# Optimization experiments

Hardware: AMD Instinct MI355X
Metric: run time of the kernel (lower is better)

Reference implementation:

```python
import jax, jax.numpy as jnp
import numpy as np

B, K, D = 131072, 1024, 128  # batch, codebook size, code dim


def setup_inputs() -> dict:
    key = jax.random.key(0)
    k1, k2 = jax.random.split(key)
    z_e = jax.random.normal(k1, (B, D), dtype=jnp.float32)
    # nn.Embedding weight init: uniform(-1/K, 1/K) as in TactileVQ.__init__
    codebook = jax.random.uniform(k2, (K, D), dtype=jnp.float32,
                                  minval=-1.0 / K, maxval=1.0 / K)
    return {"z_e": z_e, "codebook": codebook}


def reference(z_e, codebook):
    """TactileVQ forward: cdist(p=2) -> argmin -> codebook gather -> commitment MSE.
    Squared distances share the same argmin as euclidean cdist, so we use the
    expansion ||z||^2 - 2 z.E^T + ||E||^2 and never take a sqrt.
    """
    z_sq = jnp.sum(z_e * z_e, axis=-1, keepdims=True)          # [B, 1]
    e_sq = jnp.sum(codebook * codebook, axis=-1)               # [K]
    # [B, K] squared distances (monotone transform of cdist p=2)
    d2 = z_sq - 2.0 * jnp.einsum('bd,kd->bk', z_e, codebook) + e_sq
    encoding_indices = jnp.argmin(d2, axis=-1)                 # [B] int
    z_q = codebook[encoding_indices]                           # [B, D] gather
    commitment_loss = jnp.mean(
        (z_q - jax.lax.stop_gradient(z_e)) ** 2)               # mse vs detached z_e
    return z_q, commitment_loss, encoding_indices
```

## Files before the change

### kernel.cpp

```cpp
#include <hip/hip_runtime.h>
#include <math.h>

#define BN 131072
#define KN 1024
#define DN 128
#define GCODES 64
#define NGRP (KN / GCODES)

#define EROWS 64
#define EBLK (BN / EROWS)

#define ROWS 64
#define NBLK (BN / ROWS)

#define TAMB 2.5e-4f
#define CANARY 0.01f

typedef __attribute__((ext_vector_type(8))) short s16x8;
typedef __attribute__((ext_vector_type(4))) short s16x4;
typedef __attribute__((ext_vector_type(4))) float f32x4;

__device__ __forceinline__ unsigned short f2bf(float f) {
    const unsigned int u = __float_as_uint(f);
    return (unsigned short)((u + 0x7fffu + ((u >> 16) & 1u)) >> 16);
}
__device__ __forceinline__ float bf2f(unsigned short s) {
    return __uint_as_float(((unsigned int)s) << 16);
}
__device__ __forceinline__ void cvt4(const float4 v, s16x4& h4, s16x4& l4) {
    const unsigned short h0 = f2bf(v.x), h1 = f2bf(v.y), h2 = f2bf(v.z), h3 = f2bf(v.w);
    h4[0] = (short)h0; h4[1] = (short)h1; h4[2] = (short)h2; h4[3] = (short)h3;
    l4[0] = (short)f2bf(v.x - bf2f(h0));
    l4[1] = (short)f2bf(v.y - bf2f(h1));
    l4[2] = (short)f2bf(v.z - bf2f(h2));
    l4[3] = (short)f2bf(v.w - bf2f(h3));
}
__device__ __forceinline__ void cvt8(const float4 v0, const float4 v1,
                                     s16x8& h, s16x8& l) {
    s16x4 h0, l0, h1, l1;
    cvt4(v0, h0, l0); cvt4(v1, h1, l1);
    h[0]=h0[0]; h[1]=h0[1]; h[2]=h0[2]; h[3]=h0[3];
    h[4]=h1[0]; h[5]=h1[1]; h[6]=h1[2]; h[7]=h1[3];
    l[0]=l0[0]; l[1]=l0[1]; l[2]=l0[2]; l[3]=l0[3];
    l[4]=l1[0]; l[5]=l1[1]; l[6]=l1[2]; l[7]=l1[3];
}

__global__ __launch_bounds__(256) void esq_kernel(const float* __restrict__ cb,
                                                  float* __restrict__ esq) {
    int k = blockIdx.x * 256 + threadIdx.x;
    if (k >= KN) return;
    const float* row = cb + (size_t)k * DN;
    float r[8];
#pragma unroll
    for (int j = 0; j < 8; ++j) r[j] = __fmul_rn(row[j], row[j]);
#pragma unroll
    for (int i = 8; i < DN; i += 8) {
#pragma unroll
        for (int j = 0; j < 8; ++j)
            r[j] = __fadd_rn(r[j], __fmul_rn(row[i + j], row[i + j]));
    }
    esq[k] = __fadd_rn(
        __fadd_rn(__fadd_rn(r[0], r[1]), __fadd_rn(r[2], r[3])),
        __fadd_rn(__fadd_rn(r[4], r[5]), __fadd_rn(r[6], r[7])));
}

__global__ __launch_bounds__(256) void cvt_kernel(const float* __restrict__ cb,
                                                  unsigned short* __restrict__ pl) {
    const int t = blockIdx.x * 256 + threadIdx.x;
    const int g = t >> 10, rem = t & 1023;
    const int m = rem >> 6, c = rem & 63;
    const float* src = cb + ((size_t)(g * 64 + c)) * DN + m * 8;
    const float4 v0 = *reinterpret_cast<const float4*>(src);
    const float4 v1 = *reinterpret_cast<const float4*>(src + 4);
    s16x8 h, l;
    cvt8(v0, v1, h, l);
    unsigned short* hb = pl + (size_t)g * 16384 + (m * 64 + c) * 8;
    *reinterpret_cast<s16x8*>(hb)        = h;
    *reinterpret_cast<s16x8*>(hb + 8192) = l;
}

__global__ __launch_bounds__(256) void cvtT_kernel(const float* __restrict__ cb,
                                                   float* __restrict__ cbT) {
    const int idx = blockIdx.x * 256 + threadIdx.x;
    const int d = idx >> 10, k = idx & 1023;
    cbT[idx] = cb[(size_t)k * DN + d];
}

__global__ __launch_bounds__(256) void zprep_kernel(const float* __restrict__ z,
                                                    unsigned short* __restrict__ zp,
                                                    float* __restrict__ zsq) {
    const int row = blockIdx.x * 256 + threadIdx.x;
    const float* zr = z + (size_t)row * DN;
    const int gt = row >> 4, rr = row & 15;
    unsigned short* hb = zp + (size_t)gt * 4096 + rr * 8;
    float a8[8];
#pragma unroll
    for (int m = 0; m < 16; ++m) {
        const float4 v0 = *reinterpret_cast<const float4*>(zr + m * 8);
        const float4 v1 = *reinterpret_cast<const float4*>(zr + m * 8 + 4);
        s16x8 h, l;
        cvt8(v0, v1, h, l);
        *reinterpret_cast<s16x8*>(hb + m * 128)        = h;
        *reinterpret_cast<s16x8*>(hb + 2048 + m * 128) = l;
        if (m == 0) {
            a8[0] = __fmul_rn(v0.x, v0.x); a8[1] = __fmul_rn(v0.y, v0.y);
            a8[2] = __fmul_rn(v0.z, v0.z); a8[3] = __fmul_rn(v0.w, v0.w);
            a8[4] = __fmul_rn(v1.x, v1.x); a8[5] = __fmul_rn(v1.y, v1.y);
            a8[6] = __fmul_rn(v1.z, v1.z); a8[7] = __fmul_rn(v1.w, v1.w);
        } else {
            a8[0] = __fadd_rn(a8[0], __fmul_rn(v0.x, v0.x));
            a8[1] = __fadd_rn(a8[1], __fmul_rn(v0.y, v0.y));
            a8[2] = __fadd_rn(a8[2], __fmul_rn(v0.z, v0.z));
            a8[3] = __fadd_rn(a8[3], __fmul_rn(v0.w, v0.w));
            a8[4] = __fadd_rn(a8[4], __fmul_rn(v1.x, v1.x));
            a8[5] = __fadd_rn(a8[5], __fmul_rn(v1.y, v1.y));
            a8[6] = __fadd_rn(a8[6], __fmul_rn(v1.z, v1.z));
            a8[7] = __fadd_rn(a8[7], __fmul_rn(v1.w, v1.w));
        }
    }
    zsq[row] = __fadd_rn(
        __fadd_rn(__fadd_rn(a8[0], a8[1]), __fadd_rn(a8[2], a8[3])),
        __fadd_rn(__fadd_rn(a8[4], a8[5]), __fadd_rn(a8[6], a8[7])));
}

__device__ __forceinline__ float exact_d2_g(const float* __restrict__ z,
                                            const float* __restrict__ cb,
                                            const int grow, const int k,
                                            const float zsq, const float ek) {
    const float* zr = z + (size_t)grow * DN;
    const float* cr = cb + (size_t)k * DN;
    float dot = 0.0f;
#pragma unroll 4
    for (int j = 0; j < 32; ++j) {
        const float4 zv = *reinterpret_cast<const float4*>(zr + j * 4);
        const float4 cv = *reinterpret_cast<const float4*>(cr + j * 4);
        dot = __fmaf_rn(zv.x, cv.x, dot);
        dot = __fmaf_rn(zv.y, cv.y, dot);
        dot = __fmaf_rn(zv.z, cv.z, dot);
        dot = __fmaf_rn(zv.w, cv.w, dot);
    }
    return __fadd_rn(__fsub_rn(zsq, __fmul_rn(2.0f, dot)), ek);
}

__device__ __forceinline__ void tile_compute(const s16x8 (&ch)[4][4],
                                             const s16x8 (&cl)[4][4],
                                             const s16x8 (&zh)[4],
                                             const s16x8 (&zl)[4],
                                             const float (&ekv)[16],
                                             const int kbase, const int r0,
                                             float4* __restrict__ pq,
                                             const int l15, const int l4h) {
    f32x4 acc[4];
#pragma unroll
    for (int ct = 0; ct < 4; ++ct) acc[ct] = (f32x4){0.0f, 0.0f, 0.0f, 0.0f};
    __builtin_amdgcn_s_setprio(1);
#pragma unroll
    for (int ks = 0; ks < 4; ++ks) {
#pragma unroll
        for (int ct = 0; ct < 4; ++ct) {
            acc[ct] = __builtin_amdgcn_mfma_f32_16x16x32_bf16(ch[ct][ks], zh[ks], acc[ct], 0, 0, 0);
            acc[ct] = __builtin_amdgcn_mfma_f32_16x16x32_bf16(cl[ct][ks], zh[ks], acc[ct], 0, 0, 0);
            acc[ct] = __builtin_amdgcn_mfma_f32_16x16x32_bf16(ch[ct][ks], zl[ks], acc[ct], 0, 0, 0);
        }
    }
    __builtin_amdgcn_s_setprio(0);
    float b1 = INFINITY, b2 = INFINITY, b3 = INFINITY;
    int   i1 = 0, i2 = 0;
#pragma unroll
    for (int ct = 0; ct < 4; ++ct) {
#pragma unroll
        for (int e = 0; e < 4; ++e) {
            const float sc = __fmaf_rn(-2.0f, acc[ct][e], ekv[ct * 4 + e]);
            const int   kk = kbase + ct * 16 + l4h * 4 + e;
            const bool lt1 = sc < b1;
            const bool lt2 = sc < b2;
            const float nb3 = __builtin_amdgcn_fmed3f(sc, b2, b3);
            const float nb2 = __builtin_amdgcn_fmed3f(sc, b1, b2);
            i2 = lt1 ? i1 : (lt2 ? kk : i2);
            b3 = nb3;
            b2 = nb2;
            b1 = fminf(sc, b1);
            i1 = lt1 ? kk : i1;
        }
    }
#pragma unroll
    for (int st = 16; st < 64; st <<= 1) {
        const float ob1 = __shfl_xor(b1, st);
        const int   oi1 = __shfl_xor(i1, st);
        const float ob2 = __shfl_xor(b2, st);
        const int   oi2 = __shfl_xor(i2, st);
        const float ob3 = __shfl_xor(b3, st);
        float v1, v2, v3; int j1, j2;
        if (ob1 < b1) {
            v1 = ob1; j1 = oi1;
            if (b1 < ob2) { v2 = b1;  j2 = i1;  v3 = fminf(b2, ob2); }
            else          { v2 = ob2; j2 = oi2; v3 = fminf(b1, ob3); }
        } else {
            v1 = b1; j1 = i1;
            if (ob1 < b2) { v2 = ob1; j2 = oi1; v3 = fminf(ob2, b2); }
            else          { v2 = b2;  j2 = i2;  v3 = fminf(ob1, b3); }
        }
        b1 = v1; i1 = j1; b2 = v2; i2 = j2; b3 = v3;
    }
    if (l4h == 0) {
        float4 q;
        q.x = b1; q.y = b2; q.z = b3;
        q.w = __int_as_float((i2 << 16) | i1);
        pq[r0 + l15] = q;
    }
}

__device__ __forceinline__ void tile_load_zp(const unsigned short* __restrict__ zb,
                                             s16x8 (&zh)[4], s16x8 (&zl)[4]) {
#pragma unroll
    for (int ks = 0; ks < 4; ++ks) {
        zh[ks] = *reinterpret_cast<const s16x8*>(zb + ks * 512);
        zl[ks] = *reinterpret_cast<const s16x8*>(zb + 2048 + ks * 512);
    }
}

__global__ __launch_bounds__(256, 2) void vq_score_pre(const unsigned short* __restrict__ zp,
                                                       const unsigned short* __restrict__ planes,
                                                       const float* __restrict__ esq,
                                                       float4* __restrict__ pquad) {
    const int tid  = threadIdx.x;
    const int lane = tid & 63;
    const int w    = tid >> 6;
    const int l15  = lane & 15;
    const int l4h  = lane >> 4;
    const int sliceW = blockIdx.x >> 8;
    const int chunk2 = blockIdx.x & 255;
    const int sub    = sliceW * 4 + w;
    const int kbase  = sub * 64;

    s16x8 ch[4][4], cl[4][4];
    {
        const unsigned short* gp = planes + (size_t)sub * 16384;
#pragma unroll
        for (int ks = 0; ks < 4; ++ks)
#pragma unroll
            for (int ct = 0; ct < 4; ++ct) {
                const int off = ((((ks * 4 + l4h) << 6) + (ct << 4) + l15) << 3);
                ch[ct][ks] = *reinterpret_cast<const s16x8*>(gp + off);
                cl[ct][ks] = *reinterpret_cast<const s16x8*>(gp + 8192 + off);
            }
    }
    float ekv[16];
#pragma unroll
    for (int ct = 0; ct < 4; ++ct)
#pragma unroll
        for (int e = 0; e < 4; ++e)
            ekv[ct * 4 + e] = esq[kbase + ct * 16 + l4h * 4 + e];

    const int cbase = chunk2 * 32;
    const int rbase = chunk2 * 512;
    float4* pq = pquad + (size_t)sub * BN;
    const unsigned short* zpl = zp + l4h * 128 + l15 * 8;

    s16x8 hA[4], lA[4], hB[4], lB[4];
    tile_load_zp(zpl + (size_t)cbase * 4096, hA, lA);
#pragma unroll 1
    for (int t = 0; t < 32; t += 2) {
        tile_load_zp(zpl + (size_t)(cbase + t + 1) * 4096, hB, lB);
        tile_compute(ch, cl, hA, lA, ekv, kbase, rbase + t * 16, pq, l15, l4h);
        const int tn = (t + 2 < 32) ? t + 2 : 31;
        tile_load_zp(zpl + (size_t)(cbase + tn) * 4096, hA, lA);
        tile_compute(ch, cl, hB, lB, ekv, kbase, rbase + (t + 1) * 16, pq, l15, l4h);
    }
}

__global__ __launch_bounds__(256, 2) void vq_score(const float* __restrict__ z,
                                                   const unsigned short* __restrict__ planes,
                                                   const float* __restrict__ esq,
                                                   float4* __restrict__ pquad) {
    const int tid  = threadIdx.x;
    const int lane = tid & 63;
    const int w    = tid >> 6;
    const int l15  = lane & 15;
    const int l4h  = lane >> 4;
    const int sliceW = blockIdx.x >> 7;
    const int chunk  = blockIdx.x & 127;
    const int sub    = sliceW * 4 + w;
    const int kbase  = sub * 64;

    s16x8 ch[4][4], cl[4][4];
    {
        const unsigned short* gp = planes + (size_t)sub * 16384;
#pragma unroll
        for (int ks = 0; ks < 4; ++ks)
#pragma unroll
            for (int ct = 0; ct < 4; ++ct) {
                const int off = ((((ks * 4 + l4h) << 6) + (ct << 4) + l15) << 3);
                ch[ct][ks] = *reinterpret_cast<const s16x8*>(gp + off);
                cl[ct][ks] = *reinterpret_cast<const s16x8*>(gp + 8192 + off);
            }
    }
    float ekv[16];
#pragma unroll
    for (int ct = 0; ct < 4; ++ct)
#pragma unroll
        for (int e = 0; e < 4; ++e)
            ekv[ct * 4 + e] = esq[kbase + ct * 16 + l4h * 4 + e];

    const int rbase = chunk * 1024;
    float4* pq = pquad + (size_t)sub * BN;

#pragma unroll 1
    for (int t = 0; t < 64; ++t) {
        const int r0 = rbase + t * 16;
        s16x8 zh[4], zl[4];
#pragma unroll
        for (int ks = 0; ks < 4; ++ks) {
            const float* src = z + (size_t)(r0 + l15) * DN + ks * 32 + l4h * 8;
            const float4 v0 = *reinterpret_cast<const float4*>(src);
            const float4 v1 = *reinterpret_cast<const float4*>(src + 4);
            cvt8(v0, v1, zh[ks], zl[ks]);
        }
        tile_compute(ch, cl, zh, zl, ekv, kbase, r0, pq, l15, l4h);
    }
}

template <bool HZ>
__global__ __launch_bounds__(256, 2) void vq_merge3(const float* __restrict__ z,
                                                    const float* __restrict__ cb,
                                                    const float* __restrict__ esq,
                                                    const float* __restrict__ zsqArr,
                                                    const float4* __restrict__ pquad,
                                                    int* __restrict__ rmeta,
                                                    int* __restrict__ rlist,
                                                    float* __restrict__ out) {
    const int tid = threadIdx.x;
    const int r   = blockIdx.x * 256 + tid;

    float zsq;
    if constexpr (HZ) {
        zsq = zsqArr[r];
    } else {
        const float* zr = z + (size_t)r * DN;
        float a8[8];
#pragma unroll
        for (int c = 0; c < 32; ++c) {
            const float4 v = *reinterpret_cast<const float4*>(zr + c * 4);
            const int t0 = 4 * (c & 1);
            if (c < 2) {
                a8[t0 + 0] = __fmul_rn(v.x, v.x);
                a8[t0 + 1] = __fmul_rn(v.y, v.y);
                a8[t0 + 2] = __fmul_rn(v.z, v.z);
                a8[t0 + 3] = __fmul_rn(v.w, v.w);
            } else {
                a8[t0 + 0] = __fadd_rn(a8[t0 + 0], __fmul_rn(v.x, v.x));
                a8[t0 + 1] = __fadd_rn(a8[t0 + 1], __fmul_rn(v.y, v.y));
                a8[t0 + 2] = __fadd_rn(a8[t0 + 2], __fmul_rn(v.z, v.z));
                a8[t0 + 3] = __fadd_rn(a8[t0 + 3], __fmul_rn(v.w, v.w));
            }
        }
        zsq = __fadd_rn(
            __fadd_rn(__fadd_rn(a8[0], a8[1]), __fadd_rn(a8[2], a8[3])),
            __fadd_rn(__fadd_rn(a8[4], a8[5]), __fadd_rn(a8[6], a8[7])));
    }

    float B1 = INFINITY, B2 = INFINITY, B3 = INFINITY;
    int   I1 = 0, I2 = 0;
#pragma unroll
    for (int half = 0; half < 2; ++half) {
        float4 q[8];
#pragma unroll
        for (int s = 0; s < 8; ++s)
            q[s] = pquad[(size_t)(half * 8 + s) * BN + r];
#pragma unroll
        for (int s = 0; s < 8; ++s) {
            const int ii = __float_as_int(q[s].w);
            const int j1 = ii & 0xffff, j2 = ii >> 16;
            {
                const float sc = q[s].x;
                const bool lt1 = sc < B1;
                const bool lt2 = sc < B2;
                const float nB3 = __builtin_amdgcn_fmed3f(sc, B2, B3);
                const float nB2 = __builtin_amdgcn_fmed3f(sc, B1, B2);
                I2 = lt1 ? I1 : (lt2 ? j1 : I2);
                B3 = nB3;
                B2 = nB2;
                B1 = fminf(sc, B1);
                I1 = lt1 ? j1 : I1;
            }
            {
                const float sc = q[s].y;
                const bool l2 = sc < B2;
                const float nB3 = __builtin_amdgcn_fmed3f(sc, B2, B3);
                I2 = l2 ? j2 : I2;
                B3 = nB3;
                B2 = fminf(sc, B2);
            }
            B3 = fminf(B3, q[s].z);
        }
    }

    int win = I1;
    if (B3 - B1 <= TAMB) {
        const int p = atomicAdd(&rmeta[0], 1);
        rlist[p] = r;
    } else if (B2 - B1 <= TAMB) {
        const float da = exact_d2_g(z, cb, r, I1, zsq, esq[I1]);
        const float db = exact_d2_g(z, cb, r, I2, zsq, esq[I2]);
        if (da < db) win = I1;
        else if (db < da) win = I2;
        else win = (I1 < I2) ? I1 : I2;
    }
    out[(size_t)BN * DN + 1 + r] = (float)win;

    if ((tid & 63) == 0) {
        const float d2x  = exact_d2_g(z, cb, r, I1, zsq, esq[I1]);
        const float pred = __fadd_rn(zsq, B1);
        if (fabsf(pred - d2x) > CANARY) atomicExch(&rmeta[1], 1);
    }
}

template <bool HZ>
__global__ __launch_bounds__(256, 2) void vq_rescue2(const float* __restrict__ z,
                                                     const float* __restrict__ cbT,
                                                     const float* __restrict__ esq,
                                                     const float* __restrict__ zsqArr,
                                                     const int* __restrict__ rmeta,
                                                     const int* __restrict__ rlist,
                                                     float* __restrict__ out) {
    const int lane = threadIdx.x & 63;
    const int wid  = blockIdx.x * 4 + (threadIdx.x >> 6);
    const int nw   = gridDim.x * 4;
    const int n    = rmeta[0];
    const int flag = rmeta[1];
    const int total = flag ? BN : n;

    for (int ii = wid; ii < total; ii += nw) {
        const int row = flag ? ii : rlist[ii];
        float zsq;
        if constexpr (HZ) {
            zsq = zsqArr[row];
        } else {
            const float* zr0 = z + (size_t)row * DN;
            float a8[8];
#pragma unroll
            for (int c = 0; c < 32; ++c) {
                const float4 v = *reinterpret_cast<const float4*>(zr0 + c * 4);
                const int t0 = 4 * (c & 1);
                if (c < 2) {
                    a8[t0 + 0] = __fmul_rn(v.x, v.x);
                    a8[t0 + 1] = __fmul_rn(v.y, v.y);
                    a8[t0 + 2] = __fmul_rn(v.z, v.z);
                    a8[t0 + 3] = __fmul_rn(v.w, v.w);
                } else {
                    a8[t0 + 0] = __fadd_rn(a8[t0 + 0], __fmul_rn(v.x, v.x));
                    a8[t0 + 1] = __fadd_rn(a8[t0 + 1], __fmul_rn(v.y, v.y));
                    a8[t0 + 2] = __fadd_rn(a8[t0 + 2], __fmul_rn(v.z, v.z));
                    a8[t0 + 3] = __fadd_rn(a8[t0 + 3], __fmul_rn(v.w, v.w));
                }
            }
            zsq = __fadd_rn(
                __fadd_rn(__fadd_rn(a8[0], a8[1]), __fadd_rn(a8[2], a8[3])),
                __fadd_rn(__fadd_rn(a8[4], a8[5]), __fadd_rn(a8[6], a8[7])));
        }

        const float* zr = z + (size_t)row * DN;
        float acc[16];
#pragma unroll
        for (int c = 0; c < 16; ++c) acc[c] = 0.0f;
#pragma unroll 1
        for (int d = 0; d < DN; ++d) {
            const float zd = zr[d];
            const float* cd = cbT + (size_t)d * KN + lane;
#pragma unroll
            for (int c = 0; c < 16; ++c)
                acc[c] = __fmaf_rn(zd, cd[c * 64], acc[c]);
        }
        float best = INFINITY; int bi = 0;
#pragma unroll
        for (int c = 0; c < 16; ++c) {
            const int k = c * 64 + lane;
            const float d2 = __fadd_rn(__fsub_rn(zsq, __fmul_rn(2.0f, acc[c])),
                                       esq[k]);
            if (d2 < best) { best = d2; bi = k; }
        }
#pragma unroll
        for (int m = 1; m < 64; m <<= 1) {
            const float ob  = __shfl_xor(best, m);
            const int   obi = __shfl_xor(bi, m);
            if (ob < best || (ob == best && obi < bi)) { best = ob; bi = obi; }
        }
        if (lane == 0) out[(size_t)BN * DN + 1 + row] = (float)bi;
    }
}

__global__ __launch_bounds__(256, 4) void vq_epilogue(const float* __restrict__ z,
                                                      const float* __restrict__ cb,
                                                      float* __restrict__ out,
                                                      double* __restrict__ partials) {
    __shared__ int sidx[EROWS];
    __shared__ double sls[256];
    const int tid  = threadIdx.x;
    const int row0 = blockIdx.x * EROWS;

    if (tid < EROWS)
        sidx[tid] = (int)out[(size_t)BN * DN + 1 + row0 + tid];
    __syncthreads();

    double ls = 0.0;
    const int j = tid & 31;
#pragma unroll
    for (int half = 0; half < 2; ++half) {
        float4 zb[4], cv[4];
        int rr[4];
#pragma unroll
        for (int u = 0; u < 4; ++u) {
            const int it = half * 4 + u;
            rr[u] = it * 8 + (tid >> 5);
            zb[u] = *reinterpret_cast<const float4*>(
                z + (size_t)(row0 + rr[u]) * DN + j * 4);
            cv[u] = *reinterpret_cast<const float4*>(
                cb + (size_t)sidx[rr[u]] * DN + j * 4);
        }
#pragma unroll
        for (int u = 0; u < 4; ++u) {
            *reinterpret_cast<float4*>(out + (size_t)(row0 + rr[u]) * DN + j * 4) = cv[u];
            const float d0 = __fsub_rn(cv[u].x, zb[u].x);
            const float d1 = __fsub_rn(cv[u].y, zb[u].y);
            const float d2e = __fsub_rn(cv[u].z, zb[u].z);
            const float d3 = __fsub_rn(cv[u].w, zb[u].w);
            ls += (double)__fmul_rn(d0, d0);
            ls += (double)__fmul_rn(d1, d1);
            ls += (double)__fmul_rn(d2e, d2e);
            ls += (double)__fmul_rn(d3, d3);
        }
    }
    sls[tid] = ls;
    __syncthreads();
    for (int s = 128; s > 0; s >>= 1) {
        if (tid < s) sls[tid] += sls[tid + s];
        __syncthreads();
    }
    if (tid == 0) partials[blockIdx.x] = sls[0];
}

#define UPD(s, sc, kk) { \
    const bool lt1 = (sc) < b1v[s]; \
    const bool lt2 = (sc) < b2v[s]; \
    const bool lt3 = (sc) < b3v[s]; \
    b3v[s] = lt2 ? b2v[s] : (lt3 ? (sc) : b3v[s]); \
    b2v[s] = lt1 ? b1v[s] : (lt2 ? (sc) : b2v[s]); \
    i2v[s] = lt1 ? i1v[s] : (lt2 ? (kk) : i2v[s]); \
    b1v[s] = lt1 ? (sc) : b1v[s]; \
    i1v[s] = lt1 ? (kk) : i1v[s]; }

__global__ __launch_bounds__(256, 2) void vq_lds(const float* __restrict__ z,
                                                 const float* __restrict__ cb,
                                                 const float* __restrict__ esq,
                                                 float* __restrict__ out,
                                                 double* __restrict__ partials) {
    __shared__ __align__(16) short cbS[2][16384];
    __shared__ __align__(16) float sEsq[KN];
    __shared__ float  szsq[ROWS];
    __shared__ float  sB1[2][ROWS], sB2[2][ROWS], sB3[2][ROWS];
    __shared__ int    sI1[2][ROWS], sI2[2][ROWS];
    __shared__ int    sbidx[ROWS];
    __shared__ int    t2list[ROWS], t3list[ROWS];
    __shared__ int    t2n, t3n;
    __shared__ double sls[256];

    const int tid  = threadIdx.x;
    const int lane = tid & 63;
    const int w    = tid >> 6;
    const int l15  = lane & 15;
    const int l4h  = lane >> 4;
    const int wr   = w >> 1;
    const int wc   = w & 1;
    const int row0 = blockIdx.x * ROWS;

    if (tid == 0) { t2n = 0; t3n = 0; }
#pragma unroll
    for (int i = 0; i < 4; ++i) sEsq[i * 256 + tid] = esq[i * 256 + tid];

    float4 stg[8];
#pragma unroll
    for (int i = 0; i < 4; ++i) {
        const int mc = i * 256 + tid, m = mc >> 6, c = mc & 63;
        const float* src = cb + ((size_t)c) * DN + m * 8;
        stg[2 * i]     = *reinterpret_cast<const float4*>(src);
        stg[2 * i + 1] = *reinterpret_cast<const float4*>(src + 4);
    }

    if (tid < ROWS) {
        const float* zr = z + (size_t)(row0 + tid) * DN;
        float rr[8];
#pragma unroll
        for (int c = 0; c < 32; ++c) {
            const float4 v = *reinterpret_cast<const float4*>(zr + c * 4);
            const int t0 = 4 * (c & 1);
            if (c < 2) {
                rr[t0 + 0] = __fmul_rn(v.x, v.x);
                rr[t0 + 1] = __fmul_rn(v.y, v.y);
                rr[t0 + 2] = __fmul_rn(v.z, v.z);
                rr[t0 + 3] = __fmul_rn(v.w, v.w);
            } else {
                rr[t0 + 0] = __fadd_rn(rr[t0 + 0], __fmul_rn(v.x, v.x));
                rr[t0 + 1] = __fadd_rn(rr[t0 + 1], __fmul_rn(v.y, v.y));
                rr[t0 + 2] = __fadd_rn(rr[t0 + 2], __fmul_rn(v.z, v.z));
                rr[t0 + 3] = __fadd_rn(rr[t0 + 3], __fmul_rn(v.w, v.w));
            }
        }
        szsq[tid] = __fadd_rn(
            __fadd_rn(__fadd_rn(rr[0], rr[1]), __fadd_rn(rr[2], rr[3])),
            __fadd_rn(__fadd_rn(rr[4], rr[5]), __fadd_rn(rr[6], rr[7])));
    }

    {
        short* dst = &cbS[0][0];
#pragma unroll
        for (int i = 0; i < 4; ++i) {
            const int mc = i * 256 + tid, m = mc >> 6, c = mc & 63;
            s16x4 h0, l0, h1, l1;
            cvt4(stg[2 * i], h0, l0); cvt4(stg[2 * i + 1], h1, l1);
            short* hb = dst + (m * 64 + c) * 8;
            *reinterpret_cast<s16x4*>(hb)     = h0;
            *reinterpret_cast<s16x4*>(hb + 4) = h1;
            short* lb = hb + 8192;
            *reinterpret_cast<s16x4*>(lb)     = l0;
            *reinterpret_cast<s16x4*>(lb + 4) = l1;
        }
    }

    s16x8 zha[2][4], zla[2][4];
#pragma unroll
    for (int rt = 0; rt < 2; ++rt) {
#pragma unroll
        for (int ks = 0; ks < 4; ++ks) {
            const int rl = row0 + wr * 32 + rt * 16 + l15;
            const float* src = z + (size_t)rl * DN + ks * 32 + l4h * 8;
            const float4 v0 = *reinterpret_cast<const float4*>(src);
            const float4 v1 = *reinterpret_cast<const float4*>(src + 4);
            cvt8(v0, v1, zha[rt][ks], zla[rt][ks]);
        }
    }
    __syncthreads();

    float b1v[8], b2v[8], b3v[8]; int i1v[8], i2v[8];
#pragma unroll
    for (int s = 0; s < 8; ++s) {
        b1v[s] = INFINITY; b2v[s] = INFINITY; b3v[s] = INFINITY;
        i1v[s] = 0; i2v[s] = 0;
    }

    for (int g = 0; g < NGRP; ++g) {
        const int buf = g & 1;
        if (g < NGRP - 1) {
            const int gb = (g + 1) * GCODES;
#pragma unroll
            for (int i = 0; i < 4; ++i) {
                const int mc = i * 256 + tid, m = mc >> 6, c = mc & 63;
                const float* src = cb + ((size_t)(gb + c)) * DN + m * 8;
                stg[2 * i]     = *reinterpret_cast<const float4*>(src);
                stg[2 * i + 1] = *reinterpret_cast<const float4*>(src + 4);
            }
        }

        f32x4 acc[2][2];
#pragma unroll
        for (int rt = 0; rt < 2; ++rt)
#pragma unroll
            for (int ct = 0; ct < 2; ++ct)
                acc[rt][ct] = (f32x4){0.0f, 0.0f, 0.0f, 0.0f};

#pragma unroll
        for (int ks = 0; ks < 4; ++ks) {
            const int b0 = (((ks * 4 + l4h) << 6) + (wc << 5) + l15) << 3;
            const s16x8 bh0 = *reinterpret_cast<const s16x8*>(&cbS[buf][b0]);
            const s16x8 bl0 = *reinterpret_cast<const s16x8*>(&cbS[buf][8192 + b0]);
            const s16x8 bh1 = *reinterpret_cast<const s16x8*>(&cbS[buf][b0 + 128]);
            const s16x8 bl1 = *reinterpret_cast<const s16x8*>(&cbS[buf][8192 + b0 + 128]);
            acc[0][0] = __builtin_amdgcn_mfma_f32_16x16x32_bf16(zha[0][ks], bh0, acc[0][0], 0, 0, 0);
            acc[0][0] = __builtin_amdgcn_mfma_f32_16x16x32_bf16(zla[0][ks], bh0, acc[0][0], 0, 0, 0);
            acc[0][0] = __builtin_amdgcn_mfma_f32_16x16x32_bf16(zha[0][ks], bl0, acc[0][0], 0, 0, 0);
            acc[1][0] = __builtin_amdgcn_mfma_f32_16x16x32_bf16(zha[1][ks], bh0, acc[1][0], 0, 0, 0);
            acc[1][0] = __builtin_amdgcn_mfma_f32_16x16x32_bf16(zla[1][ks], bh0, acc[1][0], 0, 0, 0);
            acc[1][0] = __builtin_amdgcn_mfma_f32_16x16x32_bf16(zha[1][ks], bl0, acc[1][0], 0, 0, 0);
            acc[0][1] = __builtin_amdgcn_mfma_f32_16x16x32_bf16(zha[0][ks], bh1, acc[0][1], 0, 0, 0);
            acc[0][1] = __builtin_amdgcn_mfma_f32_16x16x32_bf16(zla[0][ks], bh1, acc[0][1], 0, 0, 0);
            acc[0][1] = __builtin_amdgcn_mfma_f32_16x16x32_bf16(zha[0][ks], bl1, acc[0][1], 0, 0, 0);
            acc[1][1] = __builtin_amdgcn_mfma_f32_16x16x32_bf16(zha[1][ks], bh1, acc[1][1], 0, 0, 0);
            acc[1][1] = __builtin_amdgcn_mfma_f32_16x16x32_bf16(zla[1][ks], bh1, acc[1][1], 0, 0, 0);
            acc[1][1] = __builtin_amdgcn_mfma_f32_16x16x32_bf16(zha[1][ks], bl1, acc[1][1], 0, 0, 0);
        }

#pragma unroll
        for (int ct = 0; ct < 2; ++ct) {
            const int k = g * GCODES + wc * 32 + ct * 16 + l15;
            const float ek = sEsq[k];
#pragma unroll
            for (int rt = 0; rt < 2; ++rt) {
#pragma unroll
                for (int e = 0; e < 4; ++e) {
                    const float sc = __fmaf_rn(-2.0f, acc[rt][ct][e], ek);
                    UPD(rt * 4 + e, sc, k)
                }
            }
        }

        if (g < NGRP - 1) {
            short* dst = &cbS[buf ^ 1][0];
#pragma unroll
            for (int i = 0; i < 4; ++i) {
                const int mc = i * 256 + tid, m = mc >> 6, c = mc & 63;
                s16x4 h0, l0, h1, l1;
                cvt4(stg[2 * i], h0, l0); cvt4(stg[2 * i + 1], h1, l1);
                short* hb = dst + (m * 64 + c) * 8;
                *reinterpret_cast<s16x4*>(hb)     = h0;
                *reinterpret_cast<s16x4*>(hb + 4) = h1;
                short* lb = hb + 8192;
                *reinterpret_cast<s16x4*>(lb)     = l0;
                *reinterpret_cast<s16x4*>(lb + 4) = l1;
            }
        }
        __syncthreads();
    }

#pragma unroll
    for (int st = 1; st < 16; st <<= 1) {
#pragma unroll
        for (int s = 0; s < 8; ++s) {
            const float ob1 = __shfl_xor(b1v[s], st);
            const int   oi1 = __shfl_xor(i1v[s], st);
            const float ob2 = __shfl_xor(b2v[s], st);
            const int   oi2 = __shfl_xor(i2v[s], st);
            const float ob3 = __shfl_xor(b3v[s], st);
            float v1, v2, v3; int j1, j2;
            if (ob1 < b1v[s]) {
                v1 = ob1; j1 = oi1;
                if (b1v[s] < ob2) { v2 = b1v[s]; j2 = i1v[s]; v3 = fminf(b2v[s], ob2); }
                else              { v2 = ob2;    j2 = oi2;    v3 = fminf(b1v[s], ob3); }
            } else {
                v1 = b1v[s]; j1 = i1v[s];
                if (ob1 < b2v[s]) { v2 = ob1;    j2 = oi1;    v3 = fminf(ob2, b2v[s]); }
                else              { v2 = b2v[s]; j2 = i2v[s]; v3 = fminf(ob1, b3v[s]); }
            }
            b1v[s] = v1; i1v[s] = j1; b2v[s] = v2; i2v[s] = j2; b3v[s] = v3;
        }
    }
    if (l15 == 0) {
#pragma unroll
        for (int s = 0; s < 8; ++s) {
            const int r = wr * 32 + (s >> 2) * 16 + l4h * 4 + (s & 3);
            sB1[wc][r] = b1v[s]; sI1[wc][r] = i1v[s];
            sB2[wc][r] = b2v[s]; sI2[wc][r] = i2v[s];
            sB3[wc][r] = b3v[s];
        }
    }
    __syncthreads();

    if (tid < ROWS) {
        const float a1 = sB1[0][tid]; const int aj1 = sI1[0][tid];
        const float a2 = sB2[0][tid]; const int aj2 = sI2[0][tid];
        const float a3 = sB3[0][tid];
        const float c1 = sB1[1][tid]; const int cj1 = sI1[1][tid];
        const float c2 = sB2[1][tid]; const int cj2 = sI2[1][tid];
        const float c3 = sB3[1][tid];
        float b1, b2, b3; int i1, i2;
        if (a1 <= c1) {
            b1 = a1; i1 = aj1;
            if (a2 <= c1) { b2 = a2; i2 = aj2; b3 = fminf(a3, c1); }
            else          { b2 = c1; i2 = cj1; b3 = fminf(a2, c2); }
        } else {
            b1 = c1; i1 = cj1;
            if (c2 <= a1) { b2 = c2; i2 = cj2; b3 = fminf(c3, a1); }
            else          { b2 = a1; i2 = aj1; b3 = fminf(c2, a2); }
        }
        sbidx[tid] = i1;
        sI1[0][tid] = i1; sI2[0][tid] = i2;
        const float d2x  = exact_d2_g(z, cb, row0 + tid, i1, szsq[tid], sEsq[i1]);
        const float pred = __fadd_rn(szsq[tid], b1);
        const bool bad   = fabsf(pred - d2x) > CANARY;
        if (bad || (b3 - b1 <= TAMB)) {
            const int p = atomicAdd(&t3n, 1); t3list[p] = tid;
        } else if (b2 - b1 <= TAMB) {
            const int p = atomicAdd(&t2n, 1); t2list[p] = tid;
        }
    }
    __syncthreads();

    if (tid < t2n) {
        const int r  = t2list[tid];
        const int ka = sI1[0][r], kb = sI2[0][r];
        const float zsq = szsq[r];
        const float da = exact_d2_g(z, cb, row0 + r, ka, zsq, sEsq[ka]);
        const float db = exact_d2_g(z, cb, row0 + r, kb, zsq, sEsq[kb]);
        int win;
        if (da < db) win = ka;
        else if (db < da) win = kb;
        else win = (ka < kb) ? ka : kb;
        sbidx[r] = win;
    }
    for (int ii = w; ii < t3n; ii += 4) {
        const int r = t3list[ii];
        const float zsq = szsq[r];
        float best = INFINITY; int bi = 0;
#pragma unroll 1
        for (int kk = 0; kk < 16; ++kk) {
            const int k = lane * 16 + kk;
            const float d2v = exact_d2_g(z, cb, row0 + r, k, zsq, sEsq[k]);
            if (d2v < best) { best = d2v; bi = k; }
        }
#pragma unroll
        for (int m = 1; m < 64; m <<= 1) {
            const float ob  = __shfl_xor(best, m);
            const int   obi = __shfl_xor(bi, m);
            if (ob < best || (ob == best && obi < bi)) { best = ob; bi = obi; }
        }
        if (lane == 0) sbidx[r] = bi;
    }
    __syncthreads();

    if (tid < ROWS)
        out[(size_t)BN * DN + 1 + row0 + tid] = (float)sbidx[tid];

    double ls = 0.0;
#pragma unroll
    for (int it = 0; it < 8; ++it) {
        const int r = it * 8 + (tid >> 5);
        const int j = tid & 31;
        const float4 zv = *reinterpret_cast<const float4*>(
            z + ((size_t)(row0 + r)) * DN + j * 4);
        const int bfin = sbidx[r];
        const float4 cv = *reinterpret_cast<const float4*>(
            cb + ((size_t)bfin) * DN + j * 4);
        *reinterpret_cast<float4*>(out + ((size_t)(row0 + r)) * DN + j * 4) = cv;
        const float d0 = __fsub_rn(cv.x, zv.x);
        const float d1 = __fsub_rn(cv.y, zv.y);
        const float d2e = __fsub_rn(cv.z, zv.z);
        const float d3 = __fsub_rn(cv.w, zv.w);
        ls += (double)__fmul_rn(d0, d0);
        ls += (double)__fmul_rn(d1, d1);
        ls += (double)__fmul_rn(d2e, d2e);
        ls += (double)__fmul_rn(d3, d3);
    }
    sls[tid] = ls;
    __syncthreads();
    for (int s = 128; s > 0; s >>= 1) {
        if (tid < s) sls[tid] += sls[tid + s];
        __syncthreads();
    }
    if (tid == 0) partials[blockIdx.x] = sls[0];
}

__global__ __launch_bounds__(256) void loss_kernel(const double* __restrict__ partials,
                                                   float* __restrict__ out, int n) {
    __shared__ double s[256];
    double acc = 0.0;
    for (int i = threadIdx.x; i < n; i += 256) acc += partials[i];
    s[threadIdx.x] = acc;
    __syncthreads();
    for (int t = 128; t > 0; t >>= 1) {
        if (threadIdx.x < t) s[threadIdx.x] += s[threadIdx.x + t];
        __syncthreads();
    }
    if (threadIdx.x == 0)
        out[(size_t)BN * DN] = (float)(s[0] / ((double)BN * (double)DN));
}

extern "C" void kernel_launch(void* const* d_in, const int* in_sizes, int n_in,
                              void* d_out, int out_size, void* d_ws, size_t ws_size,
                              hipStream_t stream) {
    const float* z  = (const float*)d_in[0];
    const float* cb = (const float*)d_in[1];
    float* out = (float*)d_out;

    float*          esq      = (float*)d_ws;
    double*         partials = (double*)((char*)d_ws + 4096);
    unsigned short* cbpl     = (unsigned short*)((char*)d_ws + 20480);
    float4*         pquad    = (float4*)((char*)d_ws + 544768);
    int*            rmeta    = (int*)((char*)d_ws + 34099200ull);
    int*            rlist    = (int*)((char*)d_ws + 34099328ull);
    float*          cbT      = (float*)((char*)d_ws + 34623616ull);
    float*          zsqArr   = (float*)((char*)d_ws + 35147904ull);
    unsigned short* zpl      = (unsigned short*)((char*)d_ws + 35672192ull);
    const size_t need_mid  = 35147904ull;
    const size_t need_full = 102781056ull;

    esq_kernel<<<KN / 256, 256, 0, stream>>>(cb, esq);
    if (ws_size >= need_full) {
        cvt_kernel  <<<64, 256, 0, stream>>>(cb, cbpl);
        cvtT_kernel <<<512, 256, 0, stream>>>(cb, cbT);
        zprep_kernel<<<BN / 256, 256, 0, stream>>>(z, zpl, zsqArr);
        vq_score_pre<<<1024, 256, 0, stream>>>(zpl, cbpl, esq, pquad);
        hipMemsetAsync(rmeta, 0, 8, stream);
        vq_merge3<true>  <<<512, 256, 0, stream>>>(z, cb, esq, zsqArr, pquad, rmeta, rlist, out);
        vq_rescue2<true> <<<512, 256, 0, stream>>>(z, cbT, esq, zsqArr, rmeta, rlist, out);
        vq_epilogue <<<EBLK, 256, 0, stream>>>(z, cb, out, partials);
        loss_kernel <<<1, 256, 0, stream>>>(partials, out, EBLK);
    } else if (ws_size >= need_mid) {
        cvt_kernel <<<64, 256, 0, stream>>>(cb, cbpl);
        cvtT_kernel<<<512, 256, 0, stream>>>(cb, cbT);
        vq_score   <<<512, 256, 0, stream>>>(z, cbpl, esq, pquad);
        hipMemsetAsync(rmeta, 0, 8, stream);
        vq_merge3<false>  <<<512, 256, 0, stream>>>(z, cb, esq, nullptr, pquad, rmeta, rlist, out);
        vq_rescue2<false> <<<512, 256, 0, stream>>>(z, cbT, esq, nullptr, rmeta, rlist, out);
        vq_epilogue<<<EBLK, 256, 0, stream>>>(z, cb, out, partials);
        loss_kernel<<<1, 256, 0, stream>>>(partials, out, EBLK);
    } else {
        vq_lds<<<NBLK, 256, 0, stream>>>(z, cb, esq, out, partials);
        loss_kernel<<<1, 256, 0, stream>>>(partials, out, NBLK);
    }
}
```

Before: 220.5 us.

## Fuse codebook prep kernels and split tier-2 rescue out of merge

Merges the esq, bf16 hi/lo split and transpose codebook prep kernels into one launch, which removes two launches. Near-tie rows with two candidates are no longer resolved with exact fp32 dot products inside the merge kernel. Merge now appends them to a new int2 list, and a separate small kernel resolves them, so merge waves no longer diverge on that work and can run at higher occupancy (launch bounds 4). The exact-distance canary check is sampled on one block in eight instead of every wave, which weakens error detection. The fallback path now also runs prep_kernel, which writes cbpl and cbT at offsets that may lie beyond a small workspace.

Result: slower. 252.7 us (+14.6%).

```diff
diff --git a/kernel.cpp b/kernel.cpp
--- a/kernel.cpp
+++ b/kernel.cpp
@@ -45,45 +45,42 @@
     l[4]=l1[0]; l[5]=l1[1]; l[6]=l1[2]; l[7]=l1[3];
 }
 
-__global__ __launch_bounds__(256) void esq_kernel(const float* __restrict__ cb,
-                                                  float* __restrict__ esq) {
-    int k = blockIdx.x * 256 + threadIdx.x;
-    if (k >= KN) return;
-    const float* row = cb + (size_t)k * DN;
-    float r[8];
-#pragma unroll
-    for (int j = 0; j < 8; ++j) r[j] = __fmul_rn(row[j], row[j]);
-#pragma unroll
-    for (int i = 8; i < DN; i += 8) {
-#pragma unroll
-        for (int j = 0; j < 8; ++j)
-            r[j] = __fadd_rn(r[j], __fmul_rn(row[i + j], row[i + j]));
-    }
-    esq[k] = __fadd_rn(
-        __fadd_rn(__fadd_rn(r[0], r[1]), __fadd_rn(r[2], r[3])),
-        __fadd_rn(__fadd_rn(r[4], r[5]), __fadd_rn(r[6], r[7])));
-}
-
-__global__ __launch_bounds__(256) void cvt_kernel(const float* __restrict__ cb,
-                                                  unsigned short* __restrict__ pl) {
-    const int t = blockIdx.x * 256 + threadIdx.x;
-    const int g = t >> 10, rem = t & 1023;
-    const int m = rem >> 6, c = rem & 63;
-    const float* src = cb + ((size_t)(g * 64 + c)) * DN + m * 8;
-    const float4 v0 = *reinterpret_cast<const float4*>(src);
-    const float4 v1 = *reinterpret_cast<const float4*>(src + 4);
-    s16x8 h, l;
-    cvt8(v0, v1, h, l);
-    unsigned short* hb = pl + (size_t)g * 16384 + (m * 64 + c) * 8;
-    *reinterpret_cast<s16x8*>(hb)        = h;
-    *reinterpret_cast<s16x8*>(hb + 8192) = l;
-}
-
-__global__ __launch_bounds__(256) void cvtT_kernel(const float* __restrict__ cb,
+__global__ __launch_bounds__(256) void prep_kernel(const float* __restrict__ cb,
+                                                   float* __restrict__ esq,
+                                                   unsigned short* __restrict__ pl,
                                                    float* __restrict__ cbT) {
     const int idx = blockIdx.x * 256 + threadIdx.x;
-    const int d = idx >> 10, k = idx & 1023;
-    cbT[idx] = cb[(size_t)k * DN + d];
+    {
+        const int d = idx >> 10, k = idx & 1023;
+        cbT[idx] = cb[(size_t)k * DN + d];
+    }
+    if (idx < 16384) {
+        const int g = idx >> 10, rem = idx & 1023;
+        const int m = rem >> 6, c = rem & 63;
+        const float* src = cb + ((size_t)(g * 64 + c)) * DN + m * 8;
+        const float4 v0 = *reinterpret_cast<const float4*>(src);
+        const float4 v1 = *reinterpret_cast<const float4*>(src + 4);
+        s16x8 h, l;
+        cvt8(v0, v1, h, l);
+        unsigned short* hb = pl + (size_t)g * 16384 + (m * 64 + c) * 8;
+        *reinterpret_cast<s16x8*>(hb)        = h;
+        *reinterpret_cast<s16x8*>(hb + 8192) = l;
+    }
+    if (idx < KN) {
+        const float* row = cb + (size_t)idx * DN;
+        float r[8];
+#pragma unroll
+        for (int j = 0; j < 8; ++j) r[j] = __fmul_rn(row[j], row[j]);
+#pragma unroll
+        for (int i = 8; i < DN; i += 8) {
+#pragma unroll
+            for (int j = 0; j < 8; ++j)
+                r[j] = __fadd_rn(r[j], __fmul_rn(row[i + j], row[i + j]));
+        }
+        esq[idx] = __fadd_rn(
+            __fadd_rn(__fadd_rn(r[0], r[1]), __fadd_rn(r[2], r[3])),
+            __fadd_rn(__fadd_rn(r[4], r[5]), __fadd_rn(r[6], r[7])));
+    }
 }
 
 __global__ __launch_bounds__(256) void zprep_kernel(const float* __restrict__ z,
@@ -142,6 +139,30 @@
     return __fadd_rn(__fsub_rn(zsq, __fmul_rn(2.0f, dot)), ek);
 }
 
+__device__ __forceinline__ float zsq_exact(const float* __restrict__ z, int row) {
+    const float* zr = z + (size_t)row * DN;
+    float a8[8];
+#pragma unroll
+    for (int c = 0; c < 32; ++c) {
+        const float4 v = *reinterpret_cast<const float4*>(zr + c * 4);
+        const int t0 = 4 * (c & 1);
+        if (c < 2) {
+            a8[t0 + 0] = __fmul_rn(v.x, v.x);
+            a8[t0 + 1] = __fmul_rn(v.y, v.y);
+            a8[t0 + 2] = __fmul_rn(v.z, v.z);
+            a8[t0 + 3] = __fmul_rn(v.w, v.w);
+        } else {
+            a8[t0 + 0] = __fadd_rn(a8[t0 + 0], __fmul_rn(v.x, v.x));
+            a8[t0 + 1] = __fadd_rn(a8[t0 + 1], __fmul_rn(v.y, v.y));
+            a8[t0 + 2] = __fadd_rn(a8[t0 + 2], __fmul_rn(v.z, v.z));
+            a8[t0 + 3] = __fadd_rn(a8[t0 + 3], __fmul_rn(v.w, v.w));
+        }
+    }
+    return __fadd_rn(
+        __fadd_rn(__fadd_rn(a8[0], a8[1]), __fadd_rn(a8[2], a8[3])),
+        __fadd_rn(__fadd_rn(a8[4], a8[5]), __fadd_rn(a8[6], a8[7])));
+}
+
 __device__ __forceinline__ void tile_compute(const s16x8 (&ch)[4][4],
                                              const s16x8 (&cl)[4][4],
                                              const s16x8 (&zh)[4],
@@ -321,43 +342,17 @@
 }
 
 template <bool HZ>
-__global__ __launch_bounds__(256, 2) void vq_merge3(const float* __restrict__ z,
+__global__ __launch_bounds__(256, 4) void vq_merge3(const float* __restrict__ z,
                                                     const float* __restrict__ cb,
                                                     const float* __restrict__ esq,
                                                     const float* __restrict__ zsqArr,
                                                     const float4* __restrict__ pquad,
                                                     int* __restrict__ rmeta,
-                                                    int* __restrict__ rlist,
+                                                    int* __restrict__ rlist3,
+                                                    int2* __restrict__ rlist2,
                                                     float* __restrict__ out) {
     const int tid = threadIdx.x;
     const int r   = blockIdx.x * 256 + tid;
-
-    float zsq;
-    if constexpr (HZ) {
-        zsq = zsqArr[r];
-    } else {
-        const float* zr = z + (size_t)r * DN;
-        float a8[8];
-#pragma unroll
-        for (int c = 0; c < 32; ++c) {
-            const float4 v = *reinterpret_cast<const float4*>(zr + c * 4);
-            const int t0 = 4 * (c & 1);
-            if (c < 2) {
-                a8[t0 + 0] = __fmul_rn(v.x, v.x);
-                a8[t0 + 1] = __fmul_rn(v.y, v.y);
-                a8[t0 + 2] = __fmul_rn(v.z, v.z);
-                a8[t0 + 3] = __fmul_rn(v.w, v.w);
-            } else {
-                a8[t0 + 0] = __fadd_rn(a8[t0 + 0], __fmul_rn(v.x, v.x));
-                a8[t0 + 1] = __fadd_rn(a8[t0 + 1], __fmul_rn(v.y, v.y));
-                a8[t0 + 2] = __fadd_rn(a8[t0 + 2], __fmul_rn(v.z, v.z));
-                a8[t0 + 3] = __fadd_rn(a8[t0 + 3], __fmul_rn(v.w, v.w));
-            }
-        }
-        zsq = __fadd_rn(
-            __fadd_rn(__fadd_rn(a8[0], a8[1]), __fadd_rn(a8[2], a8[3])),
-            __fadd_rn(__fadd_rn(a8[4], a8[5]), __fadd_rn(a8[6], a8[7])));
-    }
 
     float B1 = INFINITY, B2 = INFINITY, B3 = INFINITY;
     int   I1 = 0, I2 = 0;
@@ -395,23 +390,49 @@
         }
     }
 
-    int win = I1;
+    out[(size_t)BN * DN + 1 + r] = (float)I1;
     if (B3 - B1 <= TAMB) {
         const int p = atomicAdd(&rmeta[0], 1);
-        rlist[p] = r;
+        rlist3[p] = r;
     } else if (B2 - B1 <= TAMB) {
+        const int p = atomicAdd(&rmeta[2], 1);
+        rlist2[p] = make_int2(r, (I2 << 16) | I1);
+    }
+
+    if ((blockIdx.x & 7) == 0 && (tid & 63) == 0) {
+        float zsq;
+        if constexpr (HZ) zsq = zsqArr[r];
+        else              zsq = zsq_exact(z, r);
+        const float d2x  = exact_d2_g(z, cb, r, I1, zsq, esq[I1]);
+        const float pred = __fadd_rn(zsq, B1);
+        if (fabsf(pred - d2x) > CANARY) atomicExch(&rmeta[1], 1);
+    }
+}
+
+template <bool HZ>
+__global__ __launch_bounds__(256, 4) void vq_tier2(const float* __restrict__ z,
+                                                   const float* __restrict__ cb,
+                                                   const float* __restrict__ esq,
+                                                   const float* __restrict__ zsqArr,
+                                                   const int* __restrict__ rmeta,
+                                                   const int2* __restrict__ rlist2,
+                                                   float* __restrict__ out) {
+    const int n2 = rmeta[2];
+    for (int i = blockIdx.x * 256 + threadIdx.x; i < n2; i += gridDim.x * 256) {
+        const int2 e  = rlist2[i];
+        const int r   = e.x;
+        const int I1  = e.y & 0xffff;
+        const int I2  = e.y >> 16;
+        float zsq;
+        if constexpr (HZ) zsq = zsqArr[r];
+        else              zsq = zsq_exact(z, r);
         const float da = exact_d2_g(z, cb, r, I1, zsq, esq[I1]);
         const float db = exact_d2_g(z, cb, r, I2, zsq, esq[I2]);
+        int win;
         if (da < db) win = I1;
         else if (db < da) win = I2;
         else win = (I1 < I2) ? I1 : I2;
-    }
-    out[(size_t)BN * DN + 1 + r] = (float)win;
-
-    if ((tid & 63) == 0) {
-        const float d2x  = exact_d2_g(z, cb, r, I1, zsq, esq[I1]);
-        const float pred = __fadd_rn(zsq, B1);
-        if (fabsf(pred - d2x) > CANARY) atomicExch(&rmeta[1], 1);
+        out[(size_t)BN * DN + 1 + r] = (float)win;
     }
 }
 
@@ -421,7 +442,7 @@
                                                      const float* __restrict__ esq,
                                                      const float* __restrict__ zsqArr,
                                                      const int* __restrict__ rmeta,
-                                                     const int* __restrict__ rlist,
+                                                     const int* __restrict__ rlist3,
                                                      float* __restrict__ out) {
     const int lane = threadIdx.x & 63;
     const int wid  = blockIdx.x * 4 + (threadIdx.x >> 6);
@@ -431,33 +452,10 @@
     const int total = flag ? BN : n;
 
     for (int ii = wid; ii < total; ii += nw) {
-        const int row = flag ? ii : rlist[ii];
+        const int row = flag ? ii : rlist3[ii];
         float zsq;
-        if constexpr (HZ) {
-            zsq = zsqArr[row];
-        } else {
-            const float* zr0 = z + (size_t)row * DN;
-            float a8[8];
-#pragma unroll
-            for (int c = 0; c < 32; ++c) {
-                const float4 v = *reinterpret_cast<const float4*>(zr0 + c * 4);
-                const int t0 = 4 * (c & 1);
-                if (c < 2) {
-                    a8[t0 + 0] = __fmul_rn(v.x, v.x);
-                    a8[t0 + 1] = __fmul_rn(v.y, v.y);
-                    a8[t0 + 2] = __fmul_rn(v.z, v.z);
-                    a8[t0 + 3] = __fmul_rn(v.w, v.w);
-                } else {
-                    a8[t0 + 0] = __fadd_rn(a8[t0 + 0], __fmul_rn(v.x, v.x));
-                    a8[t0 + 1] = __fadd_rn(a8[t0 + 1], __fmul_rn(v.y, v.y));
-                    a8[t0 + 2] = __fadd_rn(a8[t0 + 2], __fmul_rn(v.z, v.z));
-                    a8[t0 + 3] = __fadd_rn(a8[t0 + 3], __fmul_rn(v.w, v.w));
-                }
-            }
-            zsq = __fadd_rn(
-                __fadd_rn(__fadd_rn(a8[0], a8[1]), __fadd_rn(a8[2], a8[3])),
-                __fadd_rn(__fadd_rn(a8[4], a8[5]), __fadd_rn(a8[6], a8[7])));
-        }
+        if constexpr (HZ) zsq = zsqArr[row];
+        else              zsq = zsq_exact(z, row);
 
         const float* zr = z + (size_t)row * DN;
         float acc[16];
@@ -586,29 +584,7 @@
         stg[2 * i + 1] = *reinterpret_cast<const float4*>(src + 4);
     }
 
-    if (tid < ROWS) {
-        const float* zr = z + (size_t)(row0 + tid) * DN;
-        float rr[8];
-#pragma unroll
-        for (int c = 0; c < 32; ++c) {
-            const float4 v = *reinterpret_cast<const float4*>(zr + c * 4);
-            const int t0 = 4 * (c & 1);
-            if (c < 2) {
-                rr[t0 + 0] = __fmul_rn(v.x, v.x);
-                rr[t0 + 1] = __fmul_rn(v.y, v.y);
-                rr[t0 + 2] = __fmul_rn(v.z, v.z);
-                rr[t0 + 3] = __fmul_rn(v.w, v.w);
-            } else {
-                rr[t0 + 0] = __fadd_rn(rr[t0 + 0], __fmul_rn(v.x, v.x));
-                rr[t0 + 1] = __fadd_rn(rr[t0 + 1], __fmul_rn(v.y, v.y));
-                rr[t0 + 2] = __fadd_rn(rr[t0 + 2], __fmul_rn(v.z, v.z));
-                rr[t0 + 3] = __fadd_rn(rr[t0 + 3], __fmul_rn(v.w, v.w));
-            }
-        }
-        szsq[tid] = __fadd_rn(
-            __fadd_rn(__fadd_rn(rr[0], rr[1]), __fadd_rn(rr[2], rr[3])),
-            __fadd_rn(__fadd_rn(rr[4], rr[5]), __fadd_rn(rr[6], rr[7])));
-    }
+    if (tid < ROWS) szsq[tid] = zsq_exact(z, row0 + tid);
 
     {
         short* dst = &cbS[0][0];
@@ -874,35 +850,37 @@
     unsigned short* cbpl     = (unsigned short*)((char*)d_ws + 20480);
     float4*         pquad    = (float4*)((char*)d_ws + 544768);
     int*            rmeta    = (int*)((char*)d_ws + 34099200ull);
-    int*            rlist    = (int*)((char*)d_ws + 34099328ull);
-    float*          cbT      = (float*)((char*)d_ws + 34623616ull);
-    float*          zsqArr   = (float*)((char*)d_ws + 35147904ull);
-    unsigned short* zpl      = (unsigned short*)((char*)d_ws + 35672192ull);
-    const size_t need_mid  = 35147904ull;
-    const size_t need_full = 102781056ull;
-
-    esq_kernel<<<KN / 256, 256, 0, stream>>>(cb, esq);
+    int*            rlist3   = (int*)((char*)d_ws + 34099328ull);
+    int2*           rlist2   = (int2*)((char*)d_ws + 34623616ull);
+    float*          cbT      = (float*)((char*)d_ws + 35672192ull);
+    float*          zsqArr   = (float*)((char*)d_ws + 36196480ull);
+    unsigned short* zpl      = (unsigned short*)((char*)d_ws + 36720768ull);
+    const size_t need_mid  = 36196480ull;
+    const size_t need_full = 103829632ull;
+
     if (ws_size >= need_full) {
-        cvt_kernel  <<<64, 256, 0, stream>>>(cb, cbpl);
-        cvtT_kernel <<<512, 256, 0, stream>>>(cb, cbT);
+        prep_kernel <<<512, 256, 0, stream>>>(cb, esq, cbpl, cbT);
         zprep_kernel<<<BN / 256, 256, 0, stream>>>(z, zpl, zsqArr);
         vq_score_pre<<<1024, 256, 0, stream>>>(zpl, cbpl, esq, pquad);
-        hipMemsetAsync(rmeta, 0, 8, stream);
-        vq_merge3<true>  <<<512, 256, 0, stream>>>(z, cb, esq, zsqArr, pquad, rmeta, rlist, out);
-        vq_rescue2<true> <<<512, 256, 0, stream>>>(z, cbT, esq, zsqArr, rmeta, rlist, out);
+        hipMemsetAsync(rmeta, 0, 12, stream);
+        vq_merge3<true>  <<<512, 256, 0, stream>>>(z, cb, esq, zsqArr, pquad, rmeta, rlist3, rlist2, out);
+        vq_tier2<true>   <<<64, 256, 0, stream>>>(z, cb, esq, zsqArr, rmeta, rlist2, out);
+        vq_rescue2<true> <<<512, 256, 0, stream>>>(z, cbT, esq, zsqArr, rmeta, rlist3, out);
         vq_epilogue <<<EBLK, 256, 0, stream>>>(z, cb, out, partials);
         loss_kernel <<<1, 256, 0, stream>>>(partials, out, EBLK);
     } else if (ws_size >= need_mid) {
-        cvt_kernel <<<64, 256, 0, stream>>>(cb, cbpl);
-        cvtT_kernel<<<512, 256, 0, stream>>>(cb, cbT);
+        prep_kernel<<<512, 256, 0, stream>>>(cb, esq, cbpl, cbT);
         vq_score   <<<512, 256, 0, stream>>>(z, cbpl, esq, pquad);
-        hipMemsetAsync(rmeta, 0, 8, stream);
-        vq_merge3<false>  <<<512, 256, 0, stream>>>(z, cb, esq, nullptr, pquad, rmeta, rlist, out);
-        vq_rescue2<false> <<<512, 256, 0, stream>>>(z, cbT, esq, nullptr, rmeta, rlist, out);
+        hipMemsetAsync(rmeta, 0, 12, stream);
+        vq_merge3<false>  <<<512, 256, 0, stream>>>(z, cb, esq, nullptr, pquad, rmeta, rlist3, rlist2, out);
+        vq_tier2<false>   <<<64, 256, 0, stream>>>(z, cb, esq, nullptr, rmeta, rlist2, out);
+        vq_rescue2<false> <<<512, 256, 0, stream>>>(z, cbT, esq, nullptr, rmeta, rlist3, out);
         vq_epilogue<<<EBLK, 256, 0, stream>>>(z, cb, out, partials);
         loss_kernel<<<1, 256, 0, stream>>>(partials, out, EBLK);
     } else {
-        vq_lds<<<NBLK, 256, 0, stream>>>(z, cb, esq, out, partials);
+        float* esq2 = (float*)d_ws;
+        prep_kernel<<<512, 256, 0, stream>>>(cb, esq2, cbpl, cbT);
+        vq_lds<<<NBLK, 256, 0, stream>>>(z, cb, esq2, out, partials);
         loss_kernel<<<1, 256, 0, stream>>>(partials, out, NBLK);
     }
 }
```
